# Optimization experiments

Hardware: AMD Instinct MI355X
Metric: run time of the kernel (lower is better)

The kernel has to match this reference:

```python
import jax, jax.numpy as jnp
import numpy as np

D = 64; T = 128; B = 64; R = 20; SEE = 10; H = 4; C = 4
N = 300000; P = 4000; K = 256


def setup_inputs() -> dict:
    key = jax.random.key(0)
    ks = jax.random.split(key, 24)
    g = lambda k, s: jax.random.normal(k, s, dtype=jnp.float32) * 0.05
    return {
        "prob_id": jax.random.randint(ks[0], (T, B), 0, P),
        "skills": jax.random.randint(ks[1], (T, B, C), 0, K),
        "response": jax.random.randint(ks[2], (T, B), 0, 2),
        "bg_index": jax.random.randint(ks[3], (T, B, R), 0, N),
        "mem_prob_ids": jax.random.randint(ks[4], (N,), 0, P),
        "mem_resp": jax.random.randint(ks[5], (N,), 0, 2),
        "mem_concepts": jax.random.randint(ks[6], (N, C), 0, K),
        "states_mem": g(ks[7], (N, D)),
        "concept_emb": g(ks[8], (K - 1, D)),
        "prob_emb": g(ks[9], (P - 1, D)),
        "W_pred": g(ks[10], (9 * D, 1)), "b_pred": jnp.zeros((1,), jnp.float32),
        "W_ih": g(ks[11], (4 * D, 3 * D)), "W_hh": g(ks[12], (D, 3 * D)),
        "b_ih": jnp.zeros((3 * D,), jnp.float32), "b_hh": jnp.zeros((3 * D,), jnp.float32),
        "W_batch": g(ks[13], (H, 3 * D, D)), "b_batch": jnp.zeros((H, D), jnp.float32),
        "W_bg": g(ks[14], (H, 3 * D, D)), "b_bg": jnp.zeros((H, D), jnp.float32),
        "W_bgint": g(ks[15], (6 * D, 6 * D)), "b_bgint": jnp.zeros((6 * D,), jnp.float32),
        "W_hisint": g(ks[16], (2 * D, 6 * D)), "b_hisint": jnp.zeros((6 * D,), jnp.float32),
        "W_inmap": g(ks[17], (10 * D, 4 * D)), "b_inmap": jnp.zeros((4 * D,), jnp.float32),
        "dir_w": g(ks[18], (2, 1)), "heads_map": g(ks[19], (H, 1)),
    }


def _forward(floats, ints):
    (states_mem, concept_emb, prob_emb, W_pred, b_pred, W_ih, W_hh, b_ih, b_hh,
     W_batch, b_batch, W_bg, b_bg, W_bgint, b_bgint, W_hisint, b_hisint,
     W_inmap, b_inmap, dir_w, heads_map) = floats
    prob_id, skills, response, bg_index, mem_prob_ids, mem_resp, mem_concepts = ints
    f32 = states_mem.dtype
    # embedding tables with zero row 0 (padding id)
    prob_cat = jnp.concatenate([jnp.zeros((1, D), f32), prob_emb], axis=0)
    conc_cat = jnp.concatenate([jnp.zeros((1, D), f32), concept_emb], axis=0)

    def prob_rep(pid, sk):
        pr = prob_cat[pid]                                     # [..., D]
        fsum = jnp.sum((sk != 0).astype(f32), axis=-1)
        div = jnp.where(fsum == 0, 1.0, fsum)[..., None]
        mean = jnp.sum(conc_cat[sk], axis=-2) / div            # masked-mean concept emb
        return jnp.concatenate([mean, pr], axis=-1)            # [..., 2D]

    dw = jax.nn.softmax(dir_w, axis=0)                          # [2,1]
    hm = heads_map[:, 0]                                        # [H]

    def step(carry, xt):
        h, h_buf, resp_buf, v_buf, t = carry
        pid, sk, resp, bgi = xt
        respf = resp.astype(f32)
        v = prob_rep(pid, sk)                                   # [B,2D]
        hidden_v = jnp.concatenate([h, v], axis=-1)             # [B,3D]
        bgi = bgi[:, :SEE]                                      # keep first see_ref refs
        bg_h = states_mem[bgi]                                  # [B,S,D] irregular gather
        bg_v = prob_rep(mem_prob_ids[bgi], mem_concepts[bgi])   # [B,S,2D]
        bg_r = mem_resp[bgi].astype(f32)[..., None]             # [B,S,1]
        all_hv = jnp.concatenate([bg_h, bg_v], axis=-1)         # [B,S,3D]
        bg_ctx = jnp.concatenate([all_hv * bg_r, all_hv * (1.0 - bg_r)], axis=-1)  # [B,S,6D]
        # multi-head attention over retrieved background states
        q = jnp.einsum('bk,hkd->bhd', hidden_v, W_batch) + b_batch[None]
        kk = jnp.einsum('bsk,hkd->bhsd', all_hv, W_bg) + b_bg[None, :, None, :]
        att = jax.nn.softmax(jnp.einsum('bhd,bhsd->bhs', q, kk) / np.sqrt(3.0 * D), axis=-1)
        heads = jnp.einsum('bhs,bsk->bhk', att, bg_ctx)          # [B,H,6D]
        bg_atts = jnp.einsum('bhk,h->bk', heads, hm)             # [B,6D]
        # attention over own history (positions 0..t valid)
        rb = resp_buf.astype(f32)[..., None]                     # [B,T+1,1]
        hr_cat = jnp.concatenate([h_buf * rb, h_buf * (1.0 - rb)], axis=-1)  # [B,T+1,2D]
        sc = jnp.einsum('bk,btk->bt', v, v_buf) / np.sqrt(2.0 * D)
        sc = jnp.where(jnp.arange(T + 1)[None, :] <= t, sc, -1e9)
        his_atts = jnp.einsum('bt,btk->bk', jax.nn.softmax(sc, axis=-1), hr_cat)  # [B,2D]
        peer = (bg_atts @ W_bgint + b_bgint) * dw[0, 0] + (his_atts @ W_hisint + b_hisint) * dw[1, 0]
        prob = (jnp.concatenate([peer, v, h], axis=-1) @ W_pred + b_pred)[:, 0]
        v_resp = jnp.concatenate([v * respf[:, None], v * (1.0 - respf[:, None])], axis=-1)
        gru_in = jnp.concatenate([peer, v_resp], axis=-1) @ W_inmap + b_inmap  # [B,4D]
        # GRU cell (torch GRUCell convention)
        gx = gru_in @ W_ih + b_ih
        gh = h @ W_hh + b_hh
        xr, xz, xn = jnp.split(gx, 3, axis=-1)
        hr, hz, hn = jnp.split(gh, 3, axis=-1)
        r = jax.nn.sigmoid(xr + hr)
        z = jax.nn.sigmoid(xz + hz)
        n = jnp.tanh(xn + r * hn)
        new_h = (1.0 - z) * n + z * h
        h_buf = h_buf.at[:, t + 1].set(new_h)
        resp_buf = resp_buf.at[:, t + 1].set(resp.astype(resp_buf.dtype))
        v_buf = v_buf.at[:, t + 1].set(v)
        return (new_h, h_buf, resp_buf, v_buf, t + 1), prob

    init = (jnp.zeros((B, D), f32), jnp.zeros((B, T + 1, D), f32),
            jnp.zeros((B, T + 1), jnp.int32), jnp.zeros((B, T + 1, 2 * D), f32),
            jnp.int32(0))
    xs = (prob_id, skills, response.astype(jnp.int32), bg_index)
    _, probs = jax.lax.scan(step, init, xs)                      # [T,B]
    return probs.T.reshape(-1)                                   # concat over batch, seq_num=T


def reference(prob_id, skills, response, bg_index, mem_prob_ids, mem_resp, mem_concepts,
              states_mem, concept_emb, prob_emb, W_pred, b_pred, W_ih, W_hh, b_ih, b_hh,
              W_batch, b_batch, W_bg, b_bg, W_bgint, b_bgint, W_hisint, b_hisint,
              W_inmap, b_inmap, dir_w, heads_map):
    floats = (states_mem, concept_emb, prob_emb, W_pred, b_pred, W_ih, W_hh, b_ih, b_hh,
              W_batch, b_batch, W_bg, b_bg, W_bgint, b_bgint, W_hisint, b_hisint,
              W_inmap, b_inmap, dir_w, heads_map)
    ints = (prob_id, skills, response, bg_index, mem_prob_ids, mem_resp, mem_concepts)
    return _forward(floats, ints)
```

## Files before the change

### kernel.cpp

```cpp
#include <hip/hip_runtime.h>
#include <hip/hip_bf16.h>

#define TT 128
#define BB 64
#define DD 64
#define RR 20
#define SEE 10
#define HH 4
#define CC 4
#define NITEM (TT*BB*SEE)
typedef __attribute__((ext_vector_type(8))) short short8;
typedef __attribute__((ext_vector_type(4))) float floatx4;

static __device__ __forceinline__ float wave_sum(float v) {
  v += __shfl_xor(v, 32); v += __shfl_xor(v, 16); v += __shfl_xor(v, 8);
  v += __shfl_xor(v, 4);  v += __shfl_xor(v, 2);  v += __shfl_xor(v, 1);
  return v;
}
static __device__ __forceinline__ float wave_max(float v) {
  v = fmaxf(v, __shfl_xor(v, 32)); v = fmaxf(v, __shfl_xor(v, 16)); v = fmaxf(v, __shfl_xor(v, 8));
  v = fmaxf(v, __shfl_xor(v, 4));  v = fmaxf(v, __shfl_xor(v, 2));  v = fmaxf(v, __shfl_xor(v, 1));
  return v;
}
static __device__ __forceinline__ unsigned short f2bf(float x) {
  __hip_bfloat16 h = __float2bfloat16(x);
  return *reinterpret_cast<unsigned short*>(&h);
}
static __device__ __forceinline__ unsigned int pack2(float lo, float hi) {
  return (unsigned int)f2bf(lo) | ((unsigned int)f2bf(hi) << 16);
}
static __device__ __forceinline__ void ldsbar() {
  asm volatile("s_waitcnt lgkmcnt(0)" ::: "memory");
  __builtin_amdgcn_s_barrier();
  asm volatile("" ::: "memory");
}

__global__ void build_v(const int* __restrict__ prob_id, const int* __restrict__ skills,
                        const float* __restrict__ concept_emb, const float* __restrict__ prob_emb,
                        float* __restrict__ V, float* __restrict__ VT) {
  int tb = blockIdx.x; int t = tb >> 6, b = tb & 63; int d = threadIdx.x;
  int pid = prob_id[tb];
  float pr = pid ? prob_emb[(pid - 1) * 64 + d] : 0.0f;
  int cnt = 0; float sum = 0.0f;
#pragma unroll
  for (int c = 0; c < 4; ++c) {
    int sk = skills[tb * 4 + c];
    if (sk) { ++cnt; sum += concept_emb[(sk - 1) * 64 + d]; }
  }
  float mean = sum / (float)(cnt ? cnt : 1);
  V[tb * 128 + d] = mean;
  V[tb * 128 + 64 + d] = pr;
  VT[b * 16384 + d * 128 + t] = mean;
  VT[b * 16384 + (64 + d) * 128 + t] = pr;
}

__global__ __launch_bounds__(256) void gemm_f32(
    const float* __restrict__ A, const float* __restrict__ B, float* __restrict__ C,
    const float* __restrict__ bias, int M, int N, int K,
    int lda, int ldb, int ldc, long sA, long sB, long sC, float scale) {
  __shared__ __align__(16) float As[64 * 36];
  __shared__ __align__(16) float Bs[32 * 64];
  const float* Ab = A + (long)blockIdx.z * sA;
  const float* Bb = B + (long)blockIdx.z * sB;
  float* Cb = C + (long)blockIdx.z * sC;
  int m0 = blockIdx.y * 64, n0 = blockIdx.x * 64;
  int tid = threadIdx.x;
  int ti = tid & 15, tj = tid >> 4;
  float acc[4][4] = {};
  for (int kc = 0; kc < K; kc += 32) {
#pragma unroll
    for (int p = 0; p < 2; ++p) {
      int q = tid + 256 * p;
      int row = q >> 3, kq = q & 7;
      *(float4*)&As[row * 36 + 4 * kq] = *(const float4*)&Ab[(size_t)(m0 + row) * lda + kc + 4 * kq];
    }
#pragma unroll
    for (int p = 0; p < 2; ++p) {
      int q = tid + 256 * p;
      int k = q >> 4, nq = q & 15;
      *(float4*)&Bs[k * 64 + 4 * nq] = *(const float4*)&Bb[(size_t)(kc + k) * ldb + n0 + 4 * nq];
    }
    __syncthreads();
#pragma unroll
    for (int k4 = 0; k4 < 8; ++k4) {
      float4 av[4], bv[4];
#pragma unroll
      for (int m = 0; m < 4; ++m) av[m] = *(const float4*)&As[(ti + 16 * m) * 36 + 4 * k4];
#pragma unroll
      for (int kk = 0; kk < 4; ++kk) bv[kk] = *(const float4*)&Bs[(4 * k4 + kk) * 64 + 4 * tj];
#pragma unroll
      for (int m = 0; m < 4; ++m) {
        const float* ap = (const float*)&av[m];
#pragma unroll
        for (int kk = 0; kk < 4; ++kk) {
          float a = ap[kk];
          acc[m][0] += a * bv[kk].x; acc[m][1] += a * bv[kk].y;
          acc[m][2] += a * bv[kk].z; acc[m][3] += a * bv[kk].w;
        }
      }
    }
    __syncthreads();
  }
  float4 bq = make_float4(0.f, 0.f, 0.f, 0.f);
  if (bias) bq = *(const float4*)&bias[n0 + 4 * tj];
#pragma unroll
  for (int m = 0; m < 4; ++m) {
    int row = m0 + ti + 16 * m;
    float4 o;
    o.x = acc[m][0] * scale + bq.x; o.y = acc[m][1] * scale + bq.y;
    o.z = acc[m][2] * scale + bq.z; o.w = acc[m][3] * scale + bq.w;
    *(float4*)&Cb[(size_t)row * ldc + n0 + 4 * tj] = o;
  }
}

__global__ __launch_bounds__(256) void k_small(
    const float* __restrict__ W_batch, const float* __restrict__ W_bg, const float* __restrict__ b_bg,
    const float* __restrict__ W_bgint, const float* __restrict__ b_bgint,
    const float* __restrict__ W_hisint, const float* __restrict__ b_hisint,
    const float* __restrict__ W_ih, const float* __restrict__ b_ih, const float* __restrict__ b_inmap,
    const float* __restrict__ W_pred, const float* __restrict__ b_pred, const float* __restrict__ dir_w,
    const float* __restrict__ M12, unsigned short* __restrict__ B1T, float* __restrict__ Hmix,
    float* __restrict__ WgT, float* __restrict__ WBvcat, float* __restrict__ Bgxv,
    float* __restrict__ c4, float* __restrict__ cgx, float* __restrict__ uh,
    float* __restrict__ bgp, float* __restrict__ c0, float* __restrict__ dwv) {
  int idx = blockIdx.x * 256 + threadIdx.x;
  const int R0 = 49152, R1 = 86016, R2 = 122880, R3 = 147456, R4 = 196608,
            R5 = 229376, R6 = 278528, R7 = 278784, R8 = 278976, R9 = 279104,
            R10 = 279488, R11 = 279489, R12 = 279491;
  if (idx < R0) {
    int k = idx >> 8, n = idx & 255; int h = n >> 6, i = n & 63;
    float s = 0.f;
    for (int d = 0; d < 64; ++d) s += W_bg[h * 12288 + k * 64 + d] * W_batch[h * 12288 + i * 64 + d];
    B1T[n * 192 + k] = f2bf(s);
  } else if (idx < R1) {
    int r = idx - R0; int k = r / 192, c = r - k * 192;
    float s = 0.f;
    for (int j = 0; j < 384; ++j) s += W_bgint[k * 384 + j] * M12[j * 192 + c];
    B1T[(256 + c) * 192 + k] = f2bf(s);
  } else if (idx < R2) {
    int r = idx - R1; int k = r / 192, c = r - k * 192;
    float s = 0.f;
    for (int j = 0; j < 384; ++j) s += W_bgint[(192 + k) * 384 + j] * M12[j * 192 + c];
    B1T[(448 + c) * 192 + k] = f2bf(s);
  } else if (idx < R3) {
    int r = idx - R2; int i = r / 192, c = r - i * 192;
    float s = 0.f;
    for (int j = 0; j < 384; ++j) s += W_hisint[i * 384 + j] * M12[j * 192 + c];
    Hmix[i * 192 + c] = s;
  } else if (idx < R4) {
    int r = idx - R3; int h = r / 12288; int rem = r - h * 12288; int d = rem / 192, k = rem - d * 192;
    WgT[r] = W_bg[h * 12288 + k * 64 + d];
  } else if (idx < R5) {
    int r = idx - R4; int i = r >> 8, n = r & 255; int h = n >> 6, d = n & 63;
    WBvcat[r] = W_batch[h * 12288 + (64 + i) * 64 + d];
  } else if (idx < R6) {
    int r = idx - R5; int i = r / 384, c = r - i * 384;
    Bgxv[r] = (c < 192) ? M12[(384 + i) * 192 + c] : M12[(512 + i) * 192 + (c - 192)];
  } else if (idx < R7) {
    int n = idx - R6; int h = n >> 6, i = n & 63;
    float s = 0.f;
    for (int d = 0; d < 64; ++d) s += W_batch[h * 12288 + i * 64 + d] * b_bg[h * 64 + d];
    c4[n] = s;
  } else if (idx < R8) {
    int c = idx - R7;
    float e0 = __expf(dir_w[0]), e1 = __expf(dir_w[1]);
    float dw0 = e0 / (e0 + e1), dw1 = e1 / (e0 + e1);
    float s = b_ih[c];
    for (int i = 0; i < 256; ++i) s += b_inmap[i] * W_ih[i * 192 + c];
    for (int k = 0; k < 384; ++k) s += (dw0 * b_bgint[k] + dw1 * b_hisint[k]) * M12[k * 192 + c];
    cgx[c] = s;
  } else if (idx < R9) {
    int i = idx - R8;
    float s = 0.f;
    for (int j = 0; j < 384; ++j) s += W_hisint[i * 384 + j] * W_pred[j];
    uh[i] = s;
  } else if (idx < R10) {
    int k = idx - R9;
    float s = 0.f;
    for (int j = 0; j < 384; ++j) s += W_bgint[k * 384 + j] * W_pred[j];
    bgp[k] = s;
  } else if (idx < R11) {
    float e0 = __expf(dir_w[0]), e1 = __expf(dir_w[1]);
    float dw0 = e0 / (e0 + e1), dw1 = e1 / (e0 + e1);
    float s = b_pred[0];
    for (int k = 0; k < 384; ++k) s += (dw0 * b_bgint[k] + dw1 * b_hisint[k]) * W_pred[k];
    c0[0] = s;
  } else if (idx < R12) {
    float e0 = __expf(dir_w[0]), e1 = __expf(dir_w[1]);
    dwv[idx - R11] = (idx == R11) ? e0 / (e0 + e1) : e1 / (e0 + e1);
  }
}

#define APAD 200
#define BPAD 40
__global__ __launch_bounds__(256) void big_gemm(
    const int* __restrict__ bg_index, const int* __restrict__ mem_prob_ids,
    const int* __restrict__ mem_resp, const int* __restrict__ mem_concepts,
    const float* __restrict__ states_mem, const float* __restrict__ concept_emb,
    const float* __restrict__ prob_emb, const unsigned short* __restrict__ B1T,
    const float* __restrict__ c4, float* __restrict__ P4s, float* __restrict__ Cg) {
  __shared__ unsigned short As[128 * APAD];
  __shared__ unsigned short Bs[128 * BPAD];
  __shared__ int bgi_l[128]; __shared__ int rf_l[128];
  int mt = blockIdx.x;
  int tid = threadIdx.x;
  int lane = tid & 63, wv = tid >> 6;
  if (tid < 128) {
    int item = mt * 128 + tid;
    int t = item / 640; int rem = item - t * 640; int b = rem / 10; int s = rem - b * 10;
    int g = bg_index[(t * 64 + b) * 20 + s];
    bgi_l[tid] = g;
    rf_l[tid] = mem_resp[g];
  }
  __syncthreads();
  {
    int half = lane >> 5;
    int hl = lane & 31;
    for (int rr = 0; rr < 32; rr += 2) {
      int r = wv * 32 + rr + half;
      int g = bgi_l[r];
      float2 sv = *(const float2*)&states_mem[g * 64 + 2 * hl];
      *(unsigned int*)&As[r * APAD + 2 * hl] = pack2(sv.x, sv.y);
      float s0 = 0.f, s1 = 0.f; int cnt = 0;
#pragma unroll
      for (int c = 0; c < 4; ++c) {
        int sk = mem_concepts[g * 4 + c];
        if (sk) { ++cnt; float2 e = *(const float2*)&concept_emb[(sk - 1) * 64 + 2 * hl]; s0 += e.x; s1 += e.y; }
      }
      float inv = 1.0f / (float)(cnt ? cnt : 1);
      *(unsigned int*)&As[r * APAD + 64 + 2 * hl] = pack2(s0 * inv, s1 * inv);
      int pid = mem_prob_ids[g];
      float2 pv = make_float2(0.f, 0.f);
      if (pid) pv = *(const float2*)&prob_emb[(pid - 1) * 64 + 2 * hl];
      *(unsigned int*)&As[r * APAD + 128 + 2 * hl] = pack2(pv.x, pv.y);
    }
  }
  int l15 = lane & 15, q = lane >> 4;
  int mh = (wv & 1) * 64, nh = (wv >> 1) * 64;
  const float invs192 = 0.07216878364870323f;
  for (int nt = 0; nt < 5; ++nt) {
    int n0 = nt * 128;
    floatx4 acc[4][4];
#pragma unroll
    for (int mi = 0; mi < 4; ++mi)
#pragma unroll
      for (int ni = 0; ni < 4; ++ni)
#pragma unroll
        for (int r = 0; r < 4; ++r) acc[mi][ni][r] = 0.f;
    for (int kc = 0; kc < 6; ++kc) {
      __syncthreads();
#pragma unroll
      for (int u = 0; u < 2; ++u) {
        int un = tid * 2 + u;
        int n = un >> 2, kk = (un & 3) * 8;
        *(float4*)&Bs[n * BPAD + kk] = *(const float4*)&B1T[(size_t)(n0 + n) * 192 + kc * 32 + kk];
      }
      __syncthreads();
      short8 a[4], bfr[4];
#pragma unroll
      for (int mi = 0; mi < 4; ++mi)
        a[mi] = *reinterpret_cast<const short8*>(&As[(mh + mi * 16 + l15) * APAD + kc * 32 + q * 8]);
#pragma unroll
      for (int ni = 0; ni < 4; ++ni)
        bfr[ni] = *reinterpret_cast<const short8*>(&Bs[(nh + ni * 16 + l15) * BPAD + q * 8]);
#pragma unroll
      for (int mi = 0; mi < 4; ++mi)
#pragma unroll
        for (int ni = 0; ni < 4; ++ni)
          acc[mi][ni] = __builtin_amdgcn_mfma_f32_16x16x32_bf16(a[mi], bfr[ni], acc[mi][ni], 0, 0, 0);
    }
    float c4v[4];
    if (n0 + nh < 256) {
#pragma unroll
      for (int ni = 0; ni < 4; ++ni) c4v[ni] = c4[n0 + nh + ni * 16 + l15];
    }
#pragma unroll
    for (int mi = 0; mi < 4; ++mi) {
#pragma unroll
      for (int r = 0; r < 4; ++r) {
        int row = mh + mi * 16 + q * 4 + r;
        int item = mt * 128 + row;
        int rf = rf_l[row];
#pragma unroll
        for (int ni = 0; ni < 4; ++ni) {
          int coln = n0 + nh + ni * 16 + l15;
          float o = acc[mi][ni][r];
          if (coln < 256) {
            P4s[(size_t)item * 256 + coln] = (o + c4v[ni]) * invs192;
          } else if (coln < 448) {
            if (rf) Cg[(size_t)item * 192 + (coln - 256)] = o;
          } else {
            if (!rf) Cg[(size_t)item * 192 + (coln - 448)] = o;
          }
        }
      }
    }
  }
}

__global__ __launch_bounds__(256) void k5(
    const int* __restrict__ bg_index, const int* __restrict__ mem_prob_ids,
    const int* __restrict__ mem_resp, const int* __restrict__ mem_concepts,
    const float* __restrict__ states_mem, const float* __restrict__ concept_emb,
    const float* __restrict__ prob_emb, const float* __restrict__ RQ, const float* __restrict__ QV,
    const float* __restrict__ b_bg, const float* __restrict__ bgp, const float* __restrict__ V,
    const float* __restrict__ W_pred, const float* __restrict__ c0,
    float* __restrict__ SQVb, float* __restrict__ cbp, float* __restrict__ PROBC) {
  int tb = blockIdx.x;
  int tid = threadIdx.x;
  int lane = tid & 63, wv = tid >> 6;
  __shared__ float ahv[10 * 196];
  __shared__ float rql[4 * 196];
  __shared__ float bgpl[384];
  __shared__ int bgi_l[10]; __shared__ int rf_s[10];
  __shared__ float cqb[4];
  if (tid < 10) { int g = bg_index[tb * 20 + tid]; bgi_l[tid] = g; rf_s[tid] = mem_resp[g]; }
  for (int i = tid; i < 384; i += 256) bgpl[i] = bgp[i];
  for (int i = tid; i < 768; i += 256) { int h = i / 192, c = i - h * 192; rql[h * 196 + c] = RQ[(size_t)tb * 768 + i]; }
  if (tid < 4) {
    float s = 0.f;
    for (int d = 0; d < 64; ++d) s += QV[tb * 256 + tid * 64 + d] * b_bg[tid * 64 + d];
    cqb[tid] = s;
  }
  __syncthreads();
  for (int s = 0; s < 10; ++s) {
    if (tid < 192) {
      int g = bgi_l[s]; float v;
      if (tid < 64) v = states_mem[g * 64 + tid];
      else if (tid < 128) {
        int d = tid - 64; float sum = 0.f; int cnt = 0;
#pragma unroll
        for (int c = 0; c < 4; ++c) { int sk = mem_concepts[g * 4 + c]; if (sk) { ++cnt; sum += concept_emb[(sk - 1) * 64 + d]; } }
        v = sum / (float)(cnt ? cnt : 1);
      } else {
        int pid = mem_prob_ids[g];
        v = pid ? prob_emb[(pid - 1) * 64 + (tid - 128)] : 0.0f;
      }
      ahv[s * 196 + tid] = v;
    }
  }
  __syncthreads();
  const float invs192 = 0.07216878364870323f;
  for (int q = 0; q < 10; ++q) {
    float v = ahv[q * 196 + lane] * rql[wv * 196 + lane]
            + ahv[q * 196 + 64 + lane] * rql[wv * 196 + 64 + lane]
            + ahv[q * 196 + 128 + lane] * rql[wv * 196 + 128 + lane];
    v = wave_sum(v);
    if (lane == 0) SQVb[tb * 40 + wv * 10 + q] = (v + cqb[wv]) * invs192;
  }
  if (wv == 0) {
    for (int q = 0; q < 10; ++q) {
      int off = rf_s[q] ? 0 : 192;
      float v = ahv[q * 196 + lane] * bgpl[off + lane]
              + ahv[q * 196 + 64 + lane] * bgpl[off + 64 + lane]
              + ahv[q * 196 + 128 + lane] * bgpl[off + 128 + lane];
      v = wave_sum(v);
      if (lane == 0) cbp[tb * 10 + q] = v;
    }
  }
  if (wv == 1) {
    float v = V[tb * 128 + lane] * W_pred[384 + lane] + V[tb * 128 + 64 + lane] * W_pred[448 + lane];
    v = wave_sum(v);
    if (lane == 0) PROBC[tb] = v + c0[0];
  }
}

__global__ __launch_bounds__(64) void prep_pw(const float* S, const int* response,
                                              float* PW, float* PR) {
  int bt = blockIdx.x; int b = bt >> 7, t = bt & 127;
  int lane = threadIdx.x;
  size_t row = (size_t)bt * 128;
  float s0 = (lane == 0) ? 0.f : ((lane <= t) ? S[row + lane - 1] : -1e30f);
  float s1 = (lane + 64 <= t) ? S[row + lane + 63] : -1e30f;
  float m = wave_max(fmaxf(s0, s1));
  float e0 = (lane <= t) ? __expf(s0 - m) : 0.f;
  float e1 = (lane + 64 <= t) ? __expf(s1 - m) : 0.f;
  float inv = 1.f / wave_sum(e0 + e1);
  float r0 = (lane >= 1) ? (float)response[(lane - 1) * 64 + b] : 0.f;
  float r1 = (float)response[(lane + 63) * 64 + b];
  PW[row + lane] = e0 * inv;
  PW[row + 64 + lane] = e1 * inv;
  PR[row + lane] = e0 * inv * r0;
  PR[row + 64 + lane] = e1 * inv * r1;
}

__global__ __launch_bounds__(512) void seq_kernel(
    const int* __restrict__ response, const float* __restrict__ P4s,
    const float* __restrict__ SQVb, const float* __restrict__ Cg,
    const float* __restrict__ GXV, const float* __restrict__ cbp,
    const float* __restrict__ PROBC, const float* __restrict__ PW,
    const float* __restrict__ PR, const float* __restrict__ Hmix,
    const float* __restrict__ W_hh, const float* __restrict__ b_hh,
    const float* __restrict__ cgx, const float* __restrict__ uh,
    const float* __restrict__ W_pred, const float* __restrict__ heads_map,
    const float* __restrict__ dwv, float* __restrict__ out) {
  int b = blockIdx.x;
  int tid = threadIdx.x;
  int lane = tid & 63, wv = tid >> 6;
  int cg3 = lane * 3;
  float hreg[16][3], wreg[8][3];
#pragma unroll
  for (int ii = 0; ii < 16; ++ii)
#pragma unroll
    for (int cc = 0; cc < 3; ++cc) hreg[ii][cc] = Hmix[(wv * 16 + ii) * 192 + cg3 + cc];
#pragma unroll
  for (int ii = 0; ii < 8; ++ii)
#pragma unroll
    for (int cc = 0; cc < 3; ++cc) wreg[ii][cc] = W_hh[(wv * 8 + ii) * 192 + cg3 + cc];
  float wph_reg[8], uh_reg[16];
  if (lane == 0) {
#pragma unroll
    for (int j = 0; j < 8; ++j) wph_reg[j] = W_pred[512 + wv * 8 + j];
#pragma unroll
    for (int ii = 0; ii < 16; ++ii) uh_reg[ii] = uh[wv * 16 + ii];
  }
  __shared__ float h_hist[128][64];
  __shared__ __align__(16) float PWl[128];
  __shared__ __align__(16) float PRl[128];
  __shared__ float h_cur[64];
  __shared__ float part_sc[8 * 40];
  __shared__ float e_l[40];
  __shared__ float ws_l[10];
  __shared__ float inv_l[4];
  __shared__ float hisA[128];
  __shared__ float red8[8][128];
  __shared__ float redWg[8][192];
  __shared__ float redWh[8][192];
  __shared__ float gh_l[192];
  __shared__ float cgx_l[192], hm_l[4];
  __shared__ float hwp_p[8], phis_p[8];
  __shared__ float phis_s, hwp_s;
  if (tid < 64) { h_cur[tid] = 0.f; h_hist[0][tid] = 0.f; }
  if (tid < 192) cgx_l[tid] = cgx[tid];
  if (tid >= 384 && tid < 388) hm_l[tid - 384] = heads_map[tid - 384];
  float dw0 = dwv[0], dw1 = dwv[1];
  int sc_off = 0;
  if (lane < 40) { int hh = lane / 10, s = lane - hh * 10; sc_off = s * 256 + hh * 64 + wv * 8; }
  float4 pfa = make_float4(0, 0, 0, 0), pfb = pfa;
  if (lane < 40) {
    pfa = *(const float4*)&P4s[(size_t)b * 2560 + sc_off];
    pfb = *(const float4*)&P4s[(size_t)b * 2560 + sc_off + 4];
  }
  float pf_sqv = 0.f;
  if (tid < 40) pf_sqv = SQVb[b * 40 + tid];
  float pf_cg0[10], pf_cg1[10], pf_cg2[10];
  float pf_gx0 = 0.f, pf_gx1 = 0.f, pf_gx2 = 0.f;
  if (tid < 64) {
#pragma unroll
    for (int s = 0; s < 10; ++s) {
      size_t base = (size_t)(b * 10 + s) * 192;
      pf_cg0[s] = Cg[base + tid]; pf_cg1[s] = Cg[base + 64 + tid]; pf_cg2[s] = Cg[base + 128 + tid];
    }
    int rn = response[b];
    size_t gb = (size_t)b * 384 + (rn ? 0 : 192);
    pf_gx0 = GXV[gb + tid]; pf_gx1 = GXV[gb + 64 + tid]; pf_gx2 = GXV[gb + 128 + tid];
  }
  float pf_cbp[10]; float pf_probc = 0.f;
  if (tid == 448) {
#pragma unroll
    for (int s = 0; s < 10; ++s) pf_cbp[s] = cbp[b * 10 + s];
    pf_probc = PROBC[b];
  }
  float4 pf_pw = make_float4(0, 0, 0, 0), pf_pr = pf_pw;
  if (tid >= 128 && tid < 160) pf_pw = *(const float4*)&PW[((size_t)(b * 128 + 0)) * 128 + 4 * (tid - 128)];
  else if (tid >= 160 && tid < 192) pf_pr = *(const float4*)&PR[((size_t)(b * 128 + 0)) * 128 + 4 * (tid - 160)];
  if (tid >= 128 && tid < 160) *(float4*)&PWl[4 * (tid - 128)] = pf_pw;
  else if (tid >= 160 && tid < 192) *(float4*)&PRl[4 * (tid - 160)] = pf_pr;
  if (tid >= 128 && tid < 160) pf_pw = *(const float4*)&PW[((size_t)(b * 128 + 1)) * 128 + 4 * (tid - 128)];
  else if (tid >= 160 && tid < 192) pf_pr = *(const float4*)&PR[((size_t)(b * 128 + 1)) * 128 + 4 * (tid - 160)];
  ldsbar();

  for (int t = 0; t < 128; ++t) {
    int tn = (t < 127) ? t + 1 : 127;
    int tbn = tn * 64 + b;
    float h_l[8];
#pragma unroll
    for (int j = 0; j < 8; ++j) h_l[j] = h_cur[wv * 8 + j];
    if (lane < 40) {
      float v = h_l[0] * pfa.x + h_l[1] * pfa.y + h_l[2] * pfa.z + h_l[3] * pfa.w
              + h_l[4] * pfb.x + h_l[5] * pfb.y + h_l[6] * pfb.z + h_l[7] * pfb.w;
      part_sc[wv * 40 + lane] = v;
      pfa = *(const float4*)&P4s[(size_t)tbn * 2560 + sc_off];
      pfb = *(const float4*)&P4s[(size_t)tbn * 2560 + sc_off + 4];
    }
    {
      float l0 = 0.f, l1 = 0.f, l2 = 0.f;
#pragma unroll
      for (int ii = 0; ii < 8; ++ii) {
        l0 += h_l[ii] * wreg[ii][0]; l1 += h_l[ii] * wreg[ii][1]; l2 += h_l[ii] * wreg[ii][2];
      }
      redWg[wv][cg3] = l0; redWg[wv][cg3 + 1] = l1; redWg[wv][cg3 + 2] = l2;
    }
    if (lane == 0) {
      float hp = 0.f;
#pragma unroll
      for (int j = 0; j < 8; ++j) hp += h_l[j] * wph_reg[j];
      hwp_p[wv] = hp;
    }
    {
      float aR = 0.f, aA = 0.f;
      for (int j = wv; j <= t; j += 8) {
        float w = PWl[j], r = PRl[j], hv = h_hist[j][lane];
        aA += w * hv; aR += r * hv;
      }
      red8[wv][lane] = aR; red8[wv][64 + lane] = aA;
    }
    ldsbar();
    if (tid < 40) {
      float s = pf_sqv;
#pragma unroll
      for (int w = 0; w < 8; ++w) s += part_sc[w * 40 + tid];
      e_l[tid] = __expf(s);
      pf_sqv = SQVb[tbn * 40 + tid];
    } else if (tid >= 64 && tid < 128) {
      int i = tid - 64;
      float sR = 0.f, sA = 0.f;
#pragma unroll
      for (int g = 0; g < 8; ++g) { sR += red8[g][i]; sA += red8[g][64 + i]; }
      hisA[i] = sR; hisA[64 + i] = sA - sR;
    } else if (tid >= 256 && tid < 448) {
      int c = tid - 256; float g = 0.f;
#pragma unroll
      for (int gg = 0; gg < 8; ++gg) g += redWg[gg][c];
      gh_l[c] = g + b_hh[c];
    } else if (tid == 450) {
      float s = 0.f;
#pragma unroll
      for (int g = 0; g < 8; ++g) s += hwp_p[g];
      hwp_s = s;
    }
    ldsbar();
    {
      float hA[16];
#pragma unroll
      for (int ii = 0; ii < 16; ++ii) hA[ii] = hisA[wv * 16 + ii];
      float l0 = 0.f, l1 = 0.f, l2 = 0.f;
#pragma unroll
      for (int ii = 0; ii < 16; ++ii) {
        l0 += hA[ii] * hreg[ii][0]; l1 += hA[ii] * hreg[ii][1]; l2 += hA[ii] * hreg[ii][2];
      }
      redWh[wv][cg3] = l0; redWh[wv][cg3 + 1] = l1; redWh[wv][cg3 + 2] = l2;
      if (lane == 0) {
        float pp = 0.f;
#pragma unroll
        for (int ii = 0; ii < 16; ++ii) pp += hA[ii] * uh_reg[ii];
        phis_p[wv] = pp;
      }
    }
    if (tid >= 452 && tid < 456) {
      int h = tid - 452;
      float den = 0.f;
#pragma unroll
      for (int s = 0; s < 10; ++s) den += e_l[h * 10 + s];
      inv_l[h] = hm_l[h] / den;
    }
    ldsbar();
    if (tid >= 256 && tid < 266) {
      int s = tid - 256;
      float w = 0.f;
#pragma unroll
      for (int h = 0; h < 4; ++h) w += inv_l[h] * e_l[h * 10 + s];
      ws_l[s] = w;
    } else if (tid == 266) {
      float p = 0.f;
#pragma unroll
      for (int g = 0; g < 8; ++g) p += phis_p[g];
      phis_s = p;
    }
    ldsbar();
    if (tid < 64) {
      float gxh0 = 0.f, gxh1 = 0.f, gxh2 = 0.f;
#pragma unroll
      for (int g = 0; g < 8; ++g) {
        gxh0 += redWh[g][tid]; gxh1 += redWh[g][64 + tid]; gxh2 += redWh[g][128 + tid];
      }
      float gbg0 = 0.f, gbg1 = 0.f, gbg2 = 0.f;
#pragma unroll
      for (int s = 0; s < 10; ++s) {
        float w = ws_l[s];
        gbg0 += w * pf_cg0[s]; gbg1 += w * pf_cg1[s]; gbg2 += w * pf_cg2[s];
      }
      float xr = dw0 * gbg0 + dw1 * gxh0 + pf_gx0 + cgx_l[tid];
      float xz = dw0 * gbg1 + dw1 * gxh1 + pf_gx1 + cgx_l[64 + tid];
      float xn = dw0 * gbg2 + dw1 * gxh2 + pf_gx2 + cgx_l[128 + tid];
      float hr = gh_l[tid], hz = gh_l[64 + tid], hn = gh_l[128 + tid];
      float r = 1.f / (1.f + __expf(-(xr + hr)));
      float z = 1.f / (1.f + __expf(-(xz + hz)));
      float n = tanhf(xn + r * hn);
      float hnew = (1.f - z) * n + z * h_cur[tid];
      h_cur[tid] = hnew;
      if (t < 127) h_hist[t + 1][tid] = hnew;
#pragma unroll
      for (int s = 0; s < 10; ++s) {
        size_t base = (size_t)(tbn * 10 + s) * 192;
        pf_cg0[s] = Cg[base + tid]; pf_cg1[s] = Cg[base + 64 + tid]; pf_cg2[s] = Cg[base + 128 + tid];
      }
      int rn = response[tbn];
      size_t gb = (size_t)tbn * 384 + (rn ? 0 : 192);
      pf_gx0 = GXV[gb + tid]; pf_gx1 = GXV[gb + 64 + tid]; pf_gx2 = GXV[gb + 128 + tid];
    } else if (tid == 448) {
      float pbg = 0.f;
#pragma unroll
      for (int s = 0; s < 10; ++s) pbg += ws_l[s] * pf_cbp[s];
      out[b * 128 + t] = dw0 * pbg + dw1 * phis_s + hwp_s + pf_probc;
#pragma unroll
      for (int s = 0; s < 10; ++s) pf_cbp[s] = cbp[tbn * 10 + s];
      pf_probc = PROBC[tbn];
    } else if (tid >= 128 && tid < 192) {
      if (tid < 160) *(float4*)&PWl[4 * (tid - 128)] = pf_pw;
      else *(float4*)&PRl[4 * (tid - 160)] = pf_pr;
      int rn2 = (t + 2 < 128) ? t + 2 : 127;
      if (tid < 160) pf_pw = *(const float4*)&PW[((size_t)(b * 128 + rn2)) * 128 + 4 * (tid - 128)];
      else pf_pr = *(const float4*)&PR[((size_t)(b * 128 + rn2)) * 128 + 4 * (tid - 160)];
    }
    ldsbar();
  }
}

extern "C" void kernel_launch(void* const* d_in, const int* in_sizes, int n_in,
                              void* d_out, int out_size, void* d_ws, size_t ws_size,
                              hipStream_t stream) {
  const int* prob_id      = (const int*)d_in[0];
  const int* skills       = (const int*)d_in[1];
  const int* response     = (const int*)d_in[2];
  const int* bg_index     = (const int*)d_in[3];
  const int* mem_prob_ids = (const int*)d_in[4];
  const int* mem_resp     = (const int*)d_in[5];
  const int* mem_concepts = (const int*)d_in[6];
  const float* states_mem  = (const float*)d_in[7];
  const float* concept_emb = (const float*)d_in[8];
  const float* prob_emb    = (const float*)d_in[9];
  const float* W_pred   = (const float*)d_in[10];
  const float* b_pred   = (const float*)d_in[11];
  const float* W_ih     = (const float*)d_in[12];
  const float* W_hh     = (const float*)d_in[13];
  const float* b_ih     = (const float*)d_in[14];
  const float* b_hh     = (const float*)d_in[15];
  const float* W_batch  = (const float*)d_in[16];
  const float* b_batch  = (const float*)d_in[17];
  const float* W_bg     = (const float*)d_in[18];
  const float* b_bg     = (const float*)d_in[19];
  const float* W_bgint  = (const float*)d_in[20];
  const float* b_bgint  = (const float*)d_in[21];
  const float* W_hisint = (const float*)d_in[22];
  const float* b_hisint = (const float*)d_in[23];
  const float* W_inmap  = (const float*)d_in[24];
  const float* b_inmap  = (const float*)d_in[25];
  const float* dir_w    = (const float*)d_in[26];
  const float* heads_map= (const float*)d_in[27];
  float* out = (float*)d_out;

  float* w = (float*)d_ws;
  size_t off = 0;
  auto alloc = [&](size_t n) { float* p = w + off; off += (n + 3) & ~(size_t)3; return p; };
  float* M12    = alloc(640 * 192);
  unsigned short* B1T = (unsigned short*)alloc(640 * 192 / 2);
  float* Hmix   = alloc(128 * 192);
  float* WgT    = alloc(4 * 192 * 64);
  float* WBvcat = alloc(128 * 256);
  float* Bgxv   = alloc(128 * 384);
  float* c4     = alloc(256);
  float* cgx    = alloc(192);
  float* uh     = alloc(128);
  float* bgp    = alloc(384);
  float* c0     = alloc(1);
  float* dwv    = alloc(2);
  float* V      = alloc((size_t)8192 * 128);
  float* VT     = alloc((size_t)64 * 128 * 128);
  float* QV     = alloc((size_t)8192 * 256);
  float* RQ     = alloc((size_t)8192 * 768);
  float* GXV    = alloc((size_t)8192 * 384);
  float* S      = alloc((size_t)64 * 128 * 128);
  float* PR     = alloc((size_t)64 * 128 * 128);
  float* P4s    = alloc((size_t)NITEM * 256);
  float* Cg     = alloc((size_t)NITEM * 192);
  float* SQVb   = alloc((size_t)8192 * 40);
  float* cbp    = alloc((size_t)NITEM);
  float* PROBC  = alloc(8192);
  (void)ws_size; (void)in_sizes; (void)n_in; (void)out_size;

  build_v<<<8192, 64, 0, stream>>>(prob_id, skills, concept_emb, prob_emb, V, VT);
  gemm_f32<<<dim3(3, 10, 1), 256, 0, stream>>>(W_inmap, W_ih, M12, nullptr,
      640, 192, 256, 256, 192, 192, 0, 0, 0, 1.0f);
  k_small<<<1092, 256, 0, stream>>>(W_batch, W_bg, b_bg, W_bgint, b_bgint, W_hisint, b_hisint,
      W_ih, b_ih, b_inmap, W_pred, b_pred, dir_w, M12, B1T, Hmix, WgT, WBvcat, Bgxv,
      c4, cgx, uh, bgp, c0, dwv);
  gemm_f32<<<dim3(4, 128, 1), 256, 0, stream>>>(V, WBvcat, QV, b_batch,
      8192, 256, 128, 128, 256, 256, 0, 0, 0, 1.0f);
  gemm_f32<<<dim3(3, 128, 4), 256, 0, stream>>>(QV, WgT, RQ, nullptr,
      8192, 192, 64, 256, 192, 768, 64, 12288, 192, 1.0f);
  gemm_f32<<<dim3(6, 128, 1), 256, 0, stream>>>(V, Bgxv, GXV, nullptr,
      8192, 384, 128, 128, 384, 384, 0, 0, 0, 1.0f);
  gemm_f32<<<dim3(2, 2, 64), 256, 0, stream>>>(V, VT, S, nullptr,
      128, 128, 128, 8192, 128, 128, 128, 16384, 16384, 0.08838834764831845f);
  prep_pw<<<8192, 64, 0, stream>>>(S, response, S, PR);
  big_gemm<<<dim3(640), 256, 0, stream>>>(bg_index, mem_prob_ids, mem_resp, mem_concepts,
      states_mem, concept_emb, prob_emb, B1T, c4, P4s, Cg);
  k5<<<8192, 256, 0, stream>>>(bg_index, mem_prob_ids, mem_resp, mem_concepts,
      states_mem, concept_emb, prob_emb, RQ, QV, b_bg, bgp, V, W_pred, c0, SQVb, cbp, PROBC);
  seq_kernel<<<64, 512, 0, stream>>>(response, P4s, SQVb, Cg, GXV, cbp, PROBC,
      S, PR, Hmix, W_hh, b_hh, cgx, uh, W_pred, heads_map, dwv, out);
}
```

Before: 872.7 us.

## Cut a barrier per step and vectorize LDS reductions in the recurrent loop

Drops one of the per-timestep block barriers: the weighted-softmax sums and the scalar partial sums are now recomputed redundantly in the GRU and output threads instead of being staged through shared memory. Shared buffers are transposed and padded so reductions and the history dot product use float4 LDS reads. The history loop becomes a fixed 16-element unrolled span per wave and no longer a t-dependent strided loop. Response values and both GX branches are prefetched so the select happens without a dependent global load, and constants move into registers. The fixed-length history sweep relies on the weights being zero beyond t; uninitialized history entries could turn into NaN if those weights are multiplied with garbage.

```diff
diff --git a/kernel.cpp b/kernel.cpp
--- a/kernel.cpp
+++ b/kernel.cpp
@@ -414,26 +414,32 @@
 #pragma unroll
     for (int ii = 0; ii < 16; ++ii) uh_reg[ii] = uh[wv * 16 + ii];
   }
-  __shared__ float h_hist[128][64];
+  float bhh_reg = 0.f;
+  if (tid >= 64 && tid < 256) bhh_reg = b_hh[tid - 64];
+  float cgx0 = 0.f, cgx1 = 0.f, cgx2 = 0.f;
+  if (tid < 64) { cgx0 = cgx[tid]; cgx1 = cgx[64 + tid]; cgx2 = cgx[128 + tid]; }
+  float hmr = 0.f;
+  if (tid >= 448 && tid < 452) hmr = heads_map[tid - 448];
+
+  __shared__ __align__(16) float h_histT[64][132];
   __shared__ __align__(16) float PWl[128];
   __shared__ __align__(16) float PRl[128];
-  __shared__ float h_cur[64];
-  __shared__ float part_sc[8 * 40];
-  __shared__ float e_l[40];
-  __shared__ float ws_l[10];
-  __shared__ float inv_l[4];
-  __shared__ float hisA[128];
-  __shared__ float red8[8][128];
+  __shared__ __align__(16) float h_cur[64];
+  __shared__ __align__(16) float part_scT[40][12];
+  __shared__ __align__(16) float e_l[40];
+  __shared__ __align__(16) float inv_l[4];
+  __shared__ __align__(16) float hisA[128];
+  __shared__ __align__(16) float red8T[128][12];
   __shared__ float redWg[8][192];
   __shared__ float redWh[8][192];
   __shared__ float gh_l[192];
-  __shared__ float cgx_l[192], hm_l[4];
   __shared__ float hwp_p[8], phis_p[8];
-  __shared__ float phis_s, hwp_s;
-  if (tid < 64) { h_cur[tid] = 0.f; h_hist[0][tid] = 0.f; }
-  if (tid < 192) cgx_l[tid] = cgx[tid];
-  if (tid >= 384 && tid < 388) hm_l[tid - 384] = heads_map[tid - 384];
+  __shared__ int resp_l[128];
+
+  if (tid < 64) { h_cur[tid] = 0.f; h_histT[tid][0] = 0.f; }
+  if (tid >= 256 && tid < 384) resp_l[tid - 256] = response[(tid - 256) * 64 + b];
   float dw0 = dwv[0], dw1 = dwv[1];
+
   int sc_off = 0;
   if (lane < 40) { int hh = lane / 10, s = lane - hh * 10; sc_off = s * 256 + hh * 64 + wv * 8; }
   float4 pfa = make_float4(0, 0, 0, 0), pfb = pfa;
@@ -442,18 +448,18 @@
     pfb = *(const float4*)&P4s[(size_t)b * 2560 + sc_off + 4];
   }
   float pf_sqv = 0.f;
-  if (tid < 40) pf_sqv = SQVb[b * 40 + tid];
+  if (tid >= 384 && tid < 424) pf_sqv = SQVb[b * 40 + (tid - 384)];
   float pf_cg0[10], pf_cg1[10], pf_cg2[10];
-  float pf_gx0 = 0.f, pf_gx1 = 0.f, pf_gx2 = 0.f;
+  float pf_gxA0 = 0.f, pf_gxA1 = 0.f, pf_gxA2 = 0.f, pf_gxB0 = 0.f, pf_gxB1 = 0.f, pf_gxB2 = 0.f;
   if (tid < 64) {
 #pragma unroll
     for (int s = 0; s < 10; ++s) {
       size_t base = (size_t)(b * 10 + s) * 192;
       pf_cg0[s] = Cg[base + tid]; pf_cg1[s] = Cg[base + 64 + tid]; pf_cg2[s] = Cg[base + 128 + tid];
     }
-    int rn = response[b];
-    size_t gb = (size_t)b * 384 + (rn ? 0 : 192);
-    pf_gx0 = GXV[gb + tid]; pf_gx1 = GXV[gb + 64 + tid]; pf_gx2 = GXV[gb + 128 + tid];
+    size_t gb = (size_t)b * 384;
+    pf_gxA0 = GXV[gb + tid]; pf_gxA1 = GXV[gb + 64 + tid]; pf_gxA2 = GXV[gb + 128 + tid];
+    pf_gxB0 = GXV[gb + 192 + tid]; pf_gxB1 = GXV[gb + 256 + tid]; pf_gxB2 = GXV[gb + 320 + tid];
   }
   float pf_cbp[10]; float pf_probc = 0.f;
   if (tid == 448) {
@@ -473,67 +479,73 @@
   for (int t = 0; t < 128; ++t) {
     int tn = (t < 127) ? t + 1 : 127;
     int tbn = tn * 64 + b;
-    float h_l[8];
-#pragma unroll
-    for (int j = 0; j < 8; ++j) h_l[j] = h_cur[wv * 8 + j];
+    float4 ha = *(const float4*)&h_cur[wv * 8];
+    float4 hb = *(const float4*)&h_cur[wv * 8 + 4];
     if (lane < 40) {
-      float v = h_l[0] * pfa.x + h_l[1] * pfa.y + h_l[2] * pfa.z + h_l[3] * pfa.w
-              + h_l[4] * pfb.x + h_l[5] * pfb.y + h_l[6] * pfb.z + h_l[7] * pfb.w;
-      part_sc[wv * 40 + lane] = v;
+      float v = ha.x * pfa.x + ha.y * pfa.y + ha.z * pfa.z + ha.w * pfa.w
+              + hb.x * pfb.x + hb.y * pfb.y + hb.z * pfb.z + hb.w * pfb.w;
+      part_scT[lane][wv] = v;
       pfa = *(const float4*)&P4s[(size_t)tbn * 2560 + sc_off];
       pfb = *(const float4*)&P4s[(size_t)tbn * 2560 + sc_off + 4];
     }
     {
+      float hl[8] = {ha.x, ha.y, ha.z, ha.w, hb.x, hb.y, hb.z, hb.w};
       float l0 = 0.f, l1 = 0.f, l2 = 0.f;
 #pragma unroll
       for (int ii = 0; ii < 8; ++ii) {
-        l0 += h_l[ii] * wreg[ii][0]; l1 += h_l[ii] * wreg[ii][1]; l2 += h_l[ii] * wreg[ii][2];
+        l0 += hl[ii] * wreg[ii][0]; l1 += hl[ii] * wreg[ii][1]; l2 += hl[ii] * wreg[ii][2];
       }
       redWg[wv][cg3] = l0; redWg[wv][cg3 + 1] = l1; redWg[wv][cg3 + 2] = l2;
-    }
-    if (lane == 0) {
-      float hp = 0.f;
-#pragma unroll
-      for (int j = 0; j < 8; ++j) hp += h_l[j] * wph_reg[j];
-      hwp_p[wv] = hp;
+      if (lane == 0) {
+        float hp = 0.f;
+#pragma unroll
+        for (int j = 0; j < 8; ++j) hp += hl[j] * wph_reg[j];
+        hwp_p[wv] = hp;
+      }
     }
     {
+      int j0 = wv * 16;
       float aR = 0.f, aA = 0.f;
-      for (int j = wv; j <= t; j += 8) {
-        float w = PWl[j], r = PRl[j], hv = h_hist[j][lane];
-        aA += w * hv; aR += r * hv;
-      }
-      red8[wv][lane] = aR; red8[wv][64 + lane] = aA;
+#pragma unroll
+      for (int k = 0; k < 4; ++k) {
+        float4 hv = *(const float4*)&h_histT[lane][j0 + 4 * k];
+        float4 w4 = *(const float4*)&PWl[j0 + 4 * k];
+        float4 r4 = *(const float4*)&PRl[j0 + 4 * k];
+        aA += w4.x * hv.x + w4.y * hv.y + w4.z * hv.z + w4.w * hv.w;
+        aR += r4.x * hv.x + r4.y * hv.y + r4.z * hv.z + r4.w * hv.w;
+      }
+      red8T[lane][wv] = aR; red8T[64 + lane][wv] = aA;
     }
     ldsbar();
-    if (tid < 40) {
-      float s = pf_sqv;
-#pragma unroll
-      for (int w = 0; w < 8; ++w) s += part_sc[w * 40 + tid];
-      e_l[tid] = __expf(s);
-      pf_sqv = SQVb[tbn * 40 + tid];
-    } else if (tid >= 64 && tid < 128) {
-      int i = tid - 64;
-      float sR = 0.f, sA = 0.f;
-#pragma unroll
-      for (int g = 0; g < 8; ++g) { sR += red8[g][i]; sA += red8[g][64 + i]; }
-      hisA[i] = sR; hisA[64 + i] = sA - sR;
-    } else if (tid >= 256 && tid < 448) {
-      int c = tid - 256; float g = 0.f;
+    if (tid < 64) {
+      float4 r0 = *(const float4*)&red8T[tid][0];
+      float4 r1 = *(const float4*)&red8T[tid][4];
+      float4 a0 = *(const float4*)&red8T[64 + tid][0];
+      float4 a1 = *(const float4*)&red8T[64 + tid][4];
+      float sR = r0.x + r0.y + r0.z + r0.w + r1.x + r1.y + r1.z + r1.w;
+      float sA = a0.x + a0.y + a0.z + a0.w + a1.x + a1.y + a1.z + a1.w;
+      hisA[tid] = sR; hisA[64 + tid] = sA - sR;
+    } else if (tid < 256) {
+      int c = tid - 64; float g = 0.f;
 #pragma unroll
       for (int gg = 0; gg < 8; ++gg) g += redWg[gg][c];
-      gh_l[c] = g + b_hh[c];
-    } else if (tid == 450) {
-      float s = 0.f;
-#pragma unroll
-      for (int g = 0; g < 8; ++g) s += hwp_p[g];
-      hwp_s = s;
+      gh_l[c] = g + bhh_reg;
+    } else if (tid >= 384 && tid < 424) {
+      int p = tid - 384;
+      float4 s0 = *(const float4*)&part_scT[p][0];
+      float4 s1 = *(const float4*)&part_scT[p][4];
+      float s = pf_sqv + s0.x + s0.y + s0.z + s0.w + s1.x + s1.y + s1.z + s1.w;
+      e_l[p] = __expf(s);
+      pf_sqv = SQVb[tbn * 40 + p];
     }
     ldsbar();
     {
-      float hA[16];
-#pragma unroll
-      for (int ii = 0; ii < 16; ++ii) hA[ii] = hisA[wv * 16 + ii];
+      float4 h0 = *(const float4*)&hisA[wv * 16];
+      float4 h1 = *(const float4*)&hisA[wv * 16 + 4];
+      float4 h2 = *(const float4*)&hisA[wv * 16 + 8];
+      float4 h3 = *(const float4*)&hisA[wv * 16 + 12];
+      float hA[16] = {h0.x, h0.y, h0.z, h0.w, h1.x, h1.y, h1.z, h1.w,
+                      h2.x, h2.y, h2.z, h2.w, h3.x, h3.y, h3.z, h3.w};
       float l0 = 0.f, l1 = 0.f, l2 = 0.f;
 #pragma unroll
       for (int ii = 0; ii < 16; ++ii) {
@@ -547,65 +559,65 @@
         phis_p[wv] = pp;
       }
     }
-    if (tid >= 452 && tid < 456) {
-      int h = tid - 452;
+    if (tid >= 448 && tid < 452) {
+      int h = tid - 448;
       float den = 0.f;
 #pragma unroll
       for (int s = 0; s < 10; ++s) den += e_l[h * 10 + s];
-      inv_l[h] = hm_l[h] / den;
+      inv_l[h] = hmr / den;
     }
     ldsbar();
-    if (tid >= 256 && tid < 266) {
-      int s = tid - 256;
-      float w = 0.f;
-#pragma unroll
-      for (int h = 0; h < 4; ++h) w += inv_l[h] * e_l[h * 10 + s];
-      ws_l[s] = w;
-    } else if (tid == 266) {
-      float p = 0.f;
-#pragma unroll
-      for (int g = 0; g < 8; ++g) p += phis_p[g];
-      phis_s = p;
-    }
-    ldsbar();
-    if (tid < 64) {
-      float gxh0 = 0.f, gxh1 = 0.f, gxh2 = 0.f;
-#pragma unroll
-      for (int g = 0; g < 8; ++g) {
-        gxh0 += redWh[g][tid]; gxh1 += redWh[g][64 + tid]; gxh2 += redWh[g][128 + tid];
-      }
-      float gbg0 = 0.f, gbg1 = 0.f, gbg2 = 0.f;
-#pragma unroll
-      for (int s = 0; s < 10; ++s) {
-        float w = ws_l[s];
-        gbg0 += w * pf_cg0[s]; gbg1 += w * pf_cg1[s]; gbg2 += w * pf_cg2[s];
-      }
-      float xr = dw0 * gbg0 + dw1 * gxh0 + pf_gx0 + cgx_l[tid];
-      float xz = dw0 * gbg1 + dw1 * gxh1 + pf_gx1 + cgx_l[64 + tid];
-      float xn = dw0 * gbg2 + dw1 * gxh2 + pf_gx2 + cgx_l[128 + tid];
-      float hr = gh_l[tid], hz = gh_l[64 + tid], hn = gh_l[128 + tid];
-      float r = 1.f / (1.f + __expf(-(xr + hr)));
-      float z = 1.f / (1.f + __expf(-(xz + hz)));
-      float n = tanhf(xn + r * hn);
-      float hnew = (1.f - z) * n + z * h_cur[tid];
-      h_cur[tid] = hnew;
-      if (t < 127) h_hist[t + 1][tid] = hnew;
-#pragma unroll
-      for (int s = 0; s < 10; ++s) {
-        size_t base = (size_t)(tbn * 10 + s) * 192;
-        pf_cg0[s] = Cg[base + tid]; pf_cg1[s] = Cg[base + 64 + tid]; pf_cg2[s] = Cg[base + 128 + tid];
-      }
-      int rn = response[tbn];
-      size_t gb = (size_t)tbn * 384 + (rn ? 0 : 192);
-      pf_gx0 = GXV[gb + tid]; pf_gx1 = GXV[gb + 64 + tid]; pf_gx2 = GXV[gb + 128 + tid];
-    } else if (tid == 448) {
-      float pbg = 0.f;
-#pragma unroll
-      for (int s = 0; s < 10; ++s) pbg += ws_l[s] * pf_cbp[s];
-      out[b * 128 + t] = dw0 * pbg + dw1 * phis_s + hwp_s + pf_probc;
-#pragma unroll
-      for (int s = 0; s < 10; ++s) pf_cbp[s] = cbp[tbn * 10 + s];
-      pf_probc = PROBC[tbn];
+    if (tid < 64 || tid == 448) {
+      float4 iv = *(const float4*)&inv_l[0];
+      float ev[40];
+#pragma unroll
+      for (int qq = 0; qq < 10; ++qq) *(float4*)&ev[4 * qq] = *(const float4*)&e_l[4 * qq];
+      float ws[10];
+#pragma unroll
+      for (int s = 0; s < 10; ++s)
+        ws[s] = iv.x * ev[s] + iv.y * ev[10 + s] + iv.z * ev[20 + s] + iv.w * ev[30 + s];
+      if (tid < 64) {
+        float gxh0 = 0.f, gxh1 = 0.f, gxh2 = 0.f;
+#pragma unroll
+        for (int g = 0; g < 8; ++g) {
+          gxh0 += redWh[g][tid]; gxh1 += redWh[g][64 + tid]; gxh2 += redWh[g][128 + tid];
+        }
+        float gbg0 = 0.f, gbg1 = 0.f, gbg2 = 0.f;
+#pragma unroll
+        for (int s = 0; s < 10; ++s) {
+          gbg0 += ws[s] * pf_cg0[s]; gbg1 += ws[s] * pf_cg1[s]; gbg2 += ws[s] * pf_cg2[s];
+        }
+        int rn = resp_l[t];
+        float xr = dw0 * gbg0 + dw1 * gxh0 + (rn ? pf_gxA0 : pf_gxB0) + cgx0;
+        float xz = dw0 * gbg1 + dw1 * gxh1 + (rn ? pf_gxA1 : pf_gxB1) + cgx1;
+        float xn = dw0 * gbg2 + dw1 * gxh2 + (rn ? pf_gxA2 : pf_gxB2) + cgx2;
+        float hr = gh_l[tid], hz = gh_l[64 + tid], hn = gh_l[128 + tid];
+        float r = 1.f / (1.f + __expf(-(xr + hr)));
+        float z = 1.f / (1.f + __expf(-(xz + hz)));
+        float n = tanhf(xn + r * hn);
+        float hnew = (1.f - z) * n + z * h_cur[tid];
+        h_cur[tid] = hnew;
+        if (t < 127) h_histT[tid][t + 1] = hnew;
+#pragma unroll
+        for (int s = 0; s < 10; ++s) {
+          size_t base = (size_t)(tbn * 10 + s) * 192;
+          pf_cg0[s] = Cg[base + tid]; pf_cg1[s] = Cg[base + 64 + tid]; pf_cg2[s] = Cg[base + 128 + tid];
+        }
+        size_t gb = (size_t)tbn * 384;
+        pf_gxA0 = GXV[gb + tid]; pf_gxA1 = GXV[gb + 64 + tid]; pf_gxA2 = GXV[gb + 128 + tid];
+        pf_gxB0 = GXV[gb + 192 + tid]; pf_gxB1 = GXV[gb + 256 + tid]; pf_gxB2 = GXV[gb + 320 + tid];
+      } else {
+        float pbg = 0.f;
+#pragma unroll
+        for (int s = 0; s < 10; ++s) pbg += ws[s] * pf_cbp[s];
+        float ph = 0.f, hw = 0.f;
+#pragma unroll
+        for (int g = 0; g < 8; ++g) { ph += phis_p[g]; hw += hwp_p[g]; }
+        out[b * 128 + t] = dw0 * pbg + dw1 * ph + hw + pf_probc;
+#pragma unroll
+        for (int s = 0; s < 10; ++s) pf_cbp[s] = cbp[tbn * 10 + s];
+        pf_probc = PROBC[tbn];
+      }
     } else if (tid >= 128 && tid < 192) {
       if (tid < 160) *(float4*)&PWl[4 * (tid - 128)] = pf_pw;
       else *(float4*)&PRl[4 * (tid - 160)] = pf_pr;
```

Measured after the change: 840.7 us. -3.7%, faster.
